# Performance work log

Hardware: AMD Instinct MI355X
Metric: run time of the kernel (lower is better)

The kernel has to match this reference:

```python
import jax, jax.numpy as jnp
import numpy as np

N, C, H, W = 4, 256, 64, 64
K, G, PAD, STRIDE, DIL = 3, 8, 1, 1, 1
GC = C // G      # channels per group
P = K * K        # sampling points per group
HIN, WIN = H + 2 * PAD, W + 2 * PAD
BN_EPS = 1e-5
LN_EPS = 1e-5


def setup_inputs():
    key = jax.random.key(0)
    ks = jax.random.split(key, 8)
    f32 = jnp.float32
    return {
        "x": jax.random.normal(ks[0], (N, C, H, W), dtype=f32),
        "w_in": jax.random.normal(ks[1], (C, C), dtype=f32) * 0.05,
        "b_in": jnp.zeros((C,), f32),
        "w_dw": jax.random.normal(ks[2], (C, 1, K, K), dtype=f32) * 0.1,
        "b_dw": jnp.zeros((C,), f32),
        "ln_g": jnp.ones((C,), f32), "ln_b": jnp.zeros((C,), f32),
        "w_off": jax.random.normal(ks[3], (C, G * P * 2), dtype=f32) * 0.01,
        "b_off": jax.random.normal(ks[4], (G * P * 2,), dtype=f32) * 0.01,
        "w_mask": jax.random.normal(ks[5], (C, G * P), dtype=f32) * 0.01,
        "b_mask": jnp.zeros((G * P,), f32),
        "w_out": jax.random.normal(ks[6], (C, C), dtype=f32) * 0.05,
        "b_out": jnp.zeros((C,), f32),
        "bn_g": jnp.ones((C,), f32), "bn_b": jnp.zeros((C,), f32),
        "bn_mean": jnp.zeros((C,), f32), "bn_var": jnp.ones((C,), f32),
    }


def _bilinear(img, grid):
    # img: (B, Cc, Hh, Ww); grid: (B, S, P, 2) normalized to [-1,1],
    # matches F.grid_sample(mode='bilinear', padding_mode='zeros', align_corners=False)
    B, Cc, Hh, Ww = img.shape
    gx = (grid[..., 0] + 1.0) * 0.5 * Ww - 0.5
    gy = (grid[..., 1] + 1.0) * 0.5 * Hh - 0.5
    x0 = jnp.floor(gx)
    y0 = jnp.floor(gy)
    wx = gx - x0
    wy = gy - y0
    flat = img.reshape(B, Cc, Hh * Ww)

    def tap(xi, yi, wgt):
        valid = (xi >= 0) & (xi <= Ww - 1) & (yi >= 0) & (yi <= Hh - 1)
        idx = (jnp.clip(yi, 0, Hh - 1) * Ww + jnp.clip(xi, 0, Ww - 1)).astype(jnp.int32)
        v = jax.vmap(lambda im, ix: im[:, ix])(flat, idx)   # (B, Cc, S, P)
        return v * (wgt * valid.astype(img.dtype))[:, None]

    return (tap(x0, y0, (1 - wx) * (1 - wy)) + tap(x0 + 1, y0, wx * (1 - wy))
            + tap(x0, y0 + 1, (1 - wx) * wy) + tap(x0 + 1, y0 + 1, wx * wy))


def _forward(x, w_in, b_in, w_dw, b_dw, ln_g, ln_b, w_off, b_off,
             w_mask, b_mask, w_out, b_out, bn_g, bn_b, bn_mean, bn_var):
    xl = jnp.transpose(x, (0, 2, 3, 1))                      # (N,H,W,C) channels-last
    x_proj = xl @ w_in + b_in                                # input_proj
    # depthwise conv + LayerNorm + GELU feature branch for offset/mask prediction
    dw = jax.lax.conv_general_dilated(
        x, w_dw, (1, 1), ((PAD, PAD), (PAD, PAD)),
        feature_group_count=C, dimension_numbers=("NCHW", "OIHW", "NCHW"))
    dw = jnp.transpose(dw + b_dw[None, :, None, None], (0, 2, 3, 1))
    mu = dw.mean(-1, keepdims=True)
    var = ((dw - mu) ** 2).mean(-1, keepdims=True)
    dw = (dw - mu) * jax.lax.rsqrt(var + LN_EPS) * ln_g + ln_b
    x1 = jax.nn.gelu(dw, approximate=False)
    offset = x1 @ w_off + b_off                              # (N,H,W,G*P*2)
    mask = jax.nn.softmax((x1 @ w_mask + b_mask).reshape(N, H, W, G, P), axis=-1)
    # reference points + dilation kernel grid, normalized to padded input, (x,y) order
    ry = ((DIL * (K - 1)) // 2 + 0.5 + jnp.arange(H, dtype=x.dtype) * STRIDE) / HIN
    rx = ((DIL * (K - 1)) // 2 + 0.5 + jnp.arange(W, dtype=x.dtype) * STRIDE) / WIN
    ref = jnp.stack(jnp.broadcast_arrays(rx[None, :], ry[:, None]), axis=-1)  # (H,W,2)
    px = (jnp.arange(K, dtype=x.dtype) * DIL - (DIL * (K - 1)) // 2) / WIN
    py = (jnp.arange(K, dtype=x.dtype) * DIL - (DIL * (K - 1)) // 2) / HIN
    gx, gy = jnp.meshgrid(px, py, indexing="ij")             # kw-major flattening as in DCNv3
    kgrid = jnp.stack([gx, gy], -1).reshape(P, 2)
    norm = jnp.array([WIN, HIN], dtype=x.dtype)
    loc = (ref[None, :, :, None, None, :] + kgrid[None, None, None, None, :, :]
           + offset.reshape(N, H, W, G, P, 2) / norm)        # (N,H,W,G,P,2), offset_scale=1
    sgrid = 2.0 * loc - 1.0
    # group-split padded value tensor and deformable sampling
    xp = jnp.pad(x_proj, ((0, 0), (PAD, PAD), (PAD, PAD), (0, 0)))
    img = jnp.transpose(xp, (0, 3, 1, 2)).reshape(N * G, GC, HIN, WIN)
    sg = jnp.transpose(sgrid.reshape(N, H * W, G, P, 2), (0, 2, 1, 3, 4)).reshape(N * G, H * W, P, 2)
    sampled = _bilinear(img, sg)                             # (N*G, GC, H*W, P)
    m = jnp.transpose(mask.reshape(N, H * W, G, P), (0, 2, 1, 3)).reshape(N * G, 1, H * W, P)
    agg = (sampled * m).sum(-1)                              # (N*G, GC, H*W)
    y = jnp.transpose(agg.reshape(N, C, H * W), (0, 2, 1)).reshape(N, H, W, C)
    y = y @ w_out + b_out                                    # output_proj
    y = jnp.transpose(y, (0, 3, 1, 2))                       # back to NCHW
    y = (y - bn_mean[None, :, None, None]) * jax.lax.rsqrt(bn_var + BN_EPS)[None, :, None, None]
    y = y * bn_g[None, :, None, None] + bn_b[None, :, None, None]
    return y * jax.nn.sigmoid(y)                             # SiLU (Conv.default_act)


def reference(x, w_in, b_in, w_dw, b_dw, ln_g, ln_b, w_off, b_off,
              w_mask, b_mask, w_out, b_out, bn_g, bn_b, bn_mean, bn_var):
    return _forward(x, w_in, b_in, w_dw, b_dw, ln_g, ln_b, w_off, b_off,
                    w_mask, b_mask, w_out, b_out, bn_g, bn_b, bn_mean, bn_var)
```

## Files before the change

kernel.cpp:

```cpp
#include <hip/hip_runtime.h>
#include <math.h>

#define NB   4
#define CCH  256
#define HH   64
#define WW   64
#define GG   8
#define GCH  32
#define PP   9
#define HIN  66
#define WIN  66
#define HWSZ 4096
#define NPIX 16384

#define XP_ELEMS   (NB*HIN*WIN*CCH)
#define AGG_ELEMS  (NPIX*CCH)
#define WINT_ELEMS (CCH*CCH)
#define WOUTT_ELEMS (CCH*CCH)
#define WOMT_ELEMS (216*CCH)
#define OFF_ELEMS  (NPIX*144)
#define MSK_ELEMS  (NPIX*72)

typedef __attribute__((ext_vector_type(8))) short bf16x8;
typedef __attribute__((ext_vector_type(4))) float f32x4;

__device__ __forceinline__ unsigned short f2bf(float f) {
    unsigned int u = __float_as_uint(f);
    unsigned int r = (u + 0x7FFFu + ((u >> 16) & 1u)) >> 16;
    return (unsigned short)r;
}
__device__ __forceinline__ float bf2f(unsigned short s) {
    return __uint_as_float(((unsigned int)s) << 16);
}

#define SDW_STRIDE 258

__global__ __launch_bounds__(256) void k_prep(
    const float* __restrict__ w_in, const float* __restrict__ w_off,
    const float* __restrict__ w_mask, const float* __restrict__ w_out,
    unsigned short* __restrict__ win_t, unsigned short* __restrict__ womt,
    unsigned short* __restrict__ wout_t, unsigned short* __restrict__ xp)
{
    const int gtid = blockIdx.x * 256 + threadIdx.x;
    const int STRIDE = 128 * 256;
    for (int i = gtid; i < 252928; i += STRIDE) {
        if (i < 65536) {
            int n = i & 255, k = i >> 8;
            win_t[n * 256 + k] = f2bf(w_in[i]);
        } else if (i < 131072) {
            int j = i - 65536;
            int n = j & 255, k = j >> 8;
            wout_t[n * 256 + k] = f2bf(w_out[j]);
        } else if (i < 186368) {
            int j = i - 131072;
            int k = j / 216, col = j - k * 216;
            float v = (col < 144) ? w_off[k * 144 + col]
                                  : w_mask[k * 72 + col - 144];
            womt[col * 256 + k] = f2bf(v);
        } else {
            int r = i - 186368;
            int seg = r >> 6, ln = r & 63;
            int n = seg / 260, rp = seg % 260;
            int h, w;
            if (rp < 66)       { h = 0;        w = rp; }
            else if (rp < 132) { h = 65;       w = rp - 66; }
            else if (rp < 196) { h = rp - 131; w = 0; }
            else               { h = rp - 195; w = 65; }
            uint2 z = make_uint2(0u, 0u);
            *(uint2*)&xp[(((size_t)n * HIN + h) * WIN + w) * CCH + ln * 4] = z;
        }
    }
}

__global__ __launch_bounds__(1024) void k_dw_fused(
    const float* __restrict__ x, const float* __restrict__ w_dw,
    const float* __restrict__ b_dw, const float* __restrict__ ln_g,
    const float* __restrict__ ln_b, const float* __restrict__ b_in,
    const unsigned short* __restrict__ win_t, const unsigned short* __restrict__ womt,
    const float* __restrict__ b_off, const float* __restrict__ b_mask,
    unsigned short* __restrict__ xp, float* __restrict__ off,
    float* __restrict__ msk)
{
    __shared__ unsigned short sdw[64 * SDW_STRIDE];
    __shared__ unsigned short sxr[64 * SDW_STRIDE];
    __shared__ float r1s[16][64];
    __shared__ float r2s[16][64];
    __shared__ float mu_s[64];
    __shared__ float rs_s[64];

    const int b = blockIdx.x;
    const int tid = threadIdx.x;
    const int h = b & 63;
    const int n = b >> 6;
    const int wave = __builtin_amdgcn_readfirstlane(tid >> 6);
    const int lane = tid & 63;

    const float* xn = x + (size_t)n * CCH * HWSZ;
    const bool h0ok = (h > 0);
    const bool h2ok = (h < HH - 1);

    float s1 = 0.f, s2 = 0.f;

#pragma unroll 4
    for (int it = 0; it < 16; it++) {
        const int c = it * 16 + wave;
        const float* xc = xn + (size_t)c * HWSZ + h * WW + lane;
        float v0 = h0ok ? xc[-WW] : 0.f;
        float v1 = xc[0];
        float v2 = h2ok ? xc[WW] : 0.f;

        const float* wk = w_dw + c * 9;
        float acc = b_dw[c];

        float l0 = __shfl_up(v0, 1);   if (lane == 0)  l0 = 0.f;
        float r0 = __shfl_down(v0, 1); if (lane == 63) r0 = 0.f;
        acc += wk[0] * l0 + wk[1] * v0 + wk[2] * r0;

        float l1 = __shfl_up(v1, 1);   if (lane == 0)  l1 = 0.f;
        float r1 = __shfl_down(v1, 1); if (lane == 63) r1 = 0.f;
        acc += wk[3] * l1 + wk[4] * v1 + wk[5] * r1;

        float l2 = __shfl_up(v2, 1);   if (lane == 0)  l2 = 0.f;
        float r2 = __shfl_down(v2, 1); if (lane == 63) r2 = 0.f;
        acc += wk[6] * l2 + wk[7] * v2 + wk[8] * r2;

        s1 += acc;
        s2 += acc * acc;
        sdw[lane * SDW_STRIDE + c] = f2bf(acc);
        sxr[lane * SDW_STRIDE + c] = f2bf(v1);
    }

    r1s[wave][lane] = s1;
    r2s[wave][lane] = s2;
    __syncthreads();

    if (tid < 64) {
        float a1 = 0.f, a2 = 0.f;
#pragma unroll
        for (int q = 0; q < 16; q++) { a1 += r1s[q][tid]; a2 += r2s[q][tid]; }
        float mu = a1 * (1.0f / 256.0f);
        float var = a2 * (1.0f / 256.0f) - mu * mu;
        mu_s[tid] = mu;
        rs_s[tid] = rsqrtf(var + 1e-5f);
    }
    __syncthreads();

    {
        const int c0 = (tid & 63) * 4;
        float g4[4], b4[4];
#pragma unroll
        for (int i = 0; i < 4; i++) { g4[i] = ln_g[c0 + i]; b4[i] = ln_b[c0 + i]; }
#pragma unroll
        for (int pass = 0; pass < 4; pass++) {
            int w = wave + pass * 16;
            float mu = mu_s[w], rs = rs_s[w];
            unsigned short* row = &sdw[w * SDW_STRIDE + c0];
#pragma unroll
            for (int i = 0; i < 4; i++) {
                float v = (bf2f(row[i]) - mu) * rs * g4[i] + b4[i];
                row[i] = f2bf(0.5f * v * (1.0f + erff(v * 0.70710678118654752f)));
            }
        }
    }
    __syncthreads();

    const int r16  = lane & 15;
    const int quad = lane >> 4;
    const int wm   = wave >> 2;
    const int wn   = wave & 3;

#define LOAD_A(frag, basep, koff)                                   \
    {                                                               \
        const unsigned short* ap_ = (basep) + (koff);               \
        ((unsigned int*)&(frag))[0] = *(const unsigned int*)&ap_[0];\
        ((unsigned int*)&(frag))[1] = *(const unsigned int*)&ap_[2];\
        ((unsigned int*)&(frag))[2] = *(const unsigned int*)&ap_[4];\
        ((unsigned int*)&(frag))[3] = *(const unsigned int*)&ap_[6];\
    }

    {
        f32x4 acc[4];
#pragma unroll
        for (int i = 0; i < 4; i++) acc[i] = (f32x4){0.f, 0.f, 0.f, 0.f};
        const unsigned short* arow = &sxr[(wm * 16 + r16) * SDW_STRIDE];

#pragma unroll
        for (int k0 = 0; k0 < CCH; k0 += 32) {
            bf16x8 a;
            LOAD_A(a, arow, k0 + quad * 8);
#pragma unroll
            for (int i = 0; i < 4; i++) {
                int co = (wn * 4 + i) * 16 + r16;
                bf16x8 bfr = *(const bf16x8*)&win_t[(size_t)co * CCH + k0 + quad * 8];
                acc[i] = __builtin_amdgcn_mfma_f32_16x16x32_bf16(a, bfr, acc[i], 0, 0, 0);
            }
        }

        unsigned short* xprow = xp + (((size_t)n * HIN + (h + 1)) * WIN + 1) * CCH;
#pragma unroll
        for (int i = 0; i < 4; i++) {
            int co = (wn * 4 + i) * 16 + r16;
            float bias = b_in[co];
#pragma unroll
            for (int r = 0; r < 4; r++) {
                int w = wm * 16 + quad * 4 + r;
                xprow[(size_t)w * CCH + co] = f2bf(acc[i][r] + bias);
            }
        }
    }

    {
        f32x4 acc[4];
#pragma unroll
        for (int i = 0; i < 4; i++) acc[i] = (f32x4){0.f, 0.f, 0.f, 0.f};
        const unsigned short* arow = &sdw[(wm * 16 + r16) * SDW_STRIDE];

#pragma unroll
        for (int k0 = 0; k0 < CCH; k0 += 32) {
            bf16x8 a;
            LOAD_A(a, arow, k0 + quad * 8);
#pragma unroll
            for (int i = 0; i < 4; i++) {
                int col = (wn * 4 + i) * 16 + r16;
                int colc = (col < 216) ? col : 215;
                bf16x8 bfr = *(const bf16x8*)&womt[(size_t)colc * CCH + k0 + quad * 8];
                acc[i] = __builtin_amdgcn_mfma_f32_16x16x32_bf16(a, bfr, acc[i], 0, 0, 0);
            }
        }

        const int sbase = n * HWSZ + h * WW;
#pragma unroll
        for (int i = 0; i < 4; i++) {
            int col = (wn * 4 + i) * 16 + r16;
            if (col >= 216) continue;
            float bias = (col < 144) ? b_off[col] : b_mask[col - 144];
#pragma unroll
            for (int r = 0; r < 4; r++) {
                int w = wm * 16 + quad * 4 + r;
                int s = sbase + w;
                float v = acc[i][r] + bias;
                if (col < 144) off[(size_t)s * 144 + col] = v;
                else           msk[(size_t)s * 72 + col - 144] = v;
            }
        }
    }
#undef LOAD_A
}

__device__ __forceinline__ void acc8_tap(float* a, uint4 vv, float wgt) {
    a[0] += wgt * __uint_as_float(vv.x << 16);
    a[1] += wgt * __uint_as_float(vv.x & 0xffff0000u);
    a[2] += wgt * __uint_as_float(vv.y << 16);
    a[3] += wgt * __uint_as_float(vv.y & 0xffff0000u);
    a[4] += wgt * __uint_as_float(vv.z << 16);
    a[5] += wgt * __uint_as_float(vv.z & 0xffff0000u);
    a[6] += wgt * __uint_as_float(vv.w << 16);
    a[7] += wgt * __uint_as_float(vv.w & 0xffff0000u);
}

__global__ __launch_bounds__(256) void k_sample_agg(
    const unsigned short* __restrict__ xp, const float* __restrict__ off,
    const float* __restrict__ msk, unsigned short* __restrict__ agg)
{
    __shared__ float  sm[576];
    __shared__ int2   tco[576];
    __shared__ float4 twt[576];

    const int tid = threadIdx.x;
    const int s0 = blockIdx.x * 8;

    if (tid < 64) {
        const int pix = tid >> 3, g = tid & 7;
        const float* mskp = msk + (size_t)(s0 + pix) * 72 + g * 9;
        float e[9];
        float mx = -1e30f;
#pragma unroll
        for (int p = 0; p < PP; p++) { e[p] = mskp[p]; mx = fmaxf(mx, e[p]); }
        float sum = 0.f;
#pragma unroll
        for (int p = 0; p < PP; p++) { e[p] = __expf(e[p] - mx); sum += e[p]; }
        float rs = 1.0f / sum;
#pragma unroll
        for (int p = 0; p < PP; p++) sm[tid * 9 + p] = e[p] * rs;
    }
    __syncthreads();

    for (int idx = tid; idx < 576; idx += 256) {
        int pix = idx / 72;
        int rem = idx - pix * 72;
        int g = rem / 9;
        int p = rem - g * 9;
        int s = s0 + pix;
        int hw = s & 4095;
        int h = hw >> 6, w = hw & 63;
        const float* offp = off + (size_t)s * 144 + g * 18 + p * 2;
        float ox = offp[0], oy = offp[1];
        int i = p / 3, j = p - i * 3;
        float fx = (float)(w + i) + ox;
        float fy = (float)(h + j) + oy;
        float x0f = floorf(fx), y0f = floorf(fy);
        int x0 = (int)x0f, y0 = (int)y0f;
        float wx = fx - x0f, wy = fy - y0f;
        float m = sm[idx];
        float w00 = (1.f - wx) * (1.f - wy) * m;
        float w10 = wx * (1.f - wy) * m;
        float w01 = (1.f - wx) * wy * m;
        float w11 = wx * wy * m;
        int x1c = x0 + 1, y1c = y0 + 1;
        if (!((x0  >= 0) && (x0  < WIN))) { w00 = 0.f; w01 = 0.f; }
        if (!((x1c >= 0) && (x1c < WIN))) { w10 = 0.f; w11 = 0.f; }
        if (!((y0  >= 0) && (y0  < HIN))) { w00 = 0.f; w10 = 0.f; }
        if (!((y1c >= 0) && (y1c < HIN))) { w01 = 0.f; w11 = 0.f; }
        int cx0 = min(max(x0, 0), WIN - 1), cx1 = min(max(x1c, 0), WIN - 1);
        int cy0 = min(max(y0, 0), HIN - 1), cy1 = min(max(y1c, 0), HIN - 1);
        tco[idx] = make_int2(cx0 | (cx1 << 16), cy0 | (cy1 << 16));
        twt[idx] = make_float4(w00, w10, w01, w11);
    }
    __syncthreads();

    const int pix = tid >> 5;
    const int l5 = tid & 31;
    const int g = l5 >> 2, c8 = l5 & 3;
    const int s = s0 + pix;
    const int n = s >> 12;
    const unsigned short* base = xp + (size_t)n * HIN * WIN * CCH + g * GCH + c8 * 8;
    const int tbase = pix * 72 + g * 9;

    float a[8];
#pragma unroll
    for (int i = 0; i < 8; i++) a[i] = 0.f;

#pragma unroll
    for (int p = 0; p < PP; p++) {
        int2 cc = tco[tbase + p];
        float4 wt = twt[tbase + p];
        int cx0 = cc.x & 0xFFFF, cx1 = cc.x >> 16;
        int cy0 = cc.y & 0xFFFF, cy1 = cc.y >> 16;
        const unsigned short* r0 = base + (size_t)(cy0 * WIN) * CCH;
        const unsigned short* r1 = base + (size_t)(cy1 * WIN) * CCH;
        uint4 v00 = *(const uint4*)&r0[(size_t)cx0 * CCH];
        uint4 v10 = *(const uint4*)&r0[(size_t)cx1 * CCH];
        uint4 v01 = *(const uint4*)&r1[(size_t)cx0 * CCH];
        uint4 v11 = *(const uint4*)&r1[(size_t)cx1 * CCH];
        acc8_tap(a, v00, wt.x);
        acc8_tap(a, v10, wt.y);
        acc8_tap(a, v01, wt.z);
        acc8_tap(a, v11, wt.w);
    }

    uint4 o;
    o.x = (unsigned int)f2bf(a[0]) | ((unsigned int)f2bf(a[1]) << 16);
    o.y = (unsigned int)f2bf(a[2]) | ((unsigned int)f2bf(a[3]) << 16);
    o.z = (unsigned int)f2bf(a[4]) | ((unsigned int)f2bf(a[5]) << 16);
    o.w = (unsigned int)f2bf(a[6]) | ((unsigned int)f2bf(a[7]) << 16);
    *(uint4*)&agg[(size_t)s * CCH + g * GCH + c8 * 8] = o;
}

__global__ __launch_bounds__(256) void k_gemm_out(
    const unsigned short* __restrict__ agg, const unsigned short* __restrict__ wout_t,
    const float* __restrict__ b_out, const float* __restrict__ bn_g,
    const float* __restrict__ bn_b, const float* __restrict__ bn_mean,
    const float* __restrict__ bn_var, float* __restrict__ out)
{
    const int m0  = blockIdx.x * 128;
    const int co0 = blockIdx.y * 64;
    const int tid = threadIdx.x;
    const int n   = m0 >> 12;
    const int hw0 = m0 & 4095;

    const int wave = tid >> 6;
    const int lane = tid & 63;
    const int r16  = lane & 15;
    const int quad = lane >> 4;
    const int mw   = wave * 32;

    f32x4 acc[2][4];
#pragma unroll
    for (int i = 0; i < 2; i++)
#pragma unroll
        for (int j = 0; j < 4; j++) acc[i][j] = (f32x4){0.f, 0.f, 0.f, 0.f};

    const unsigned short* a0p = agg + (size_t)(m0 + mw + r16) * CCH + quad * 8;
    const unsigned short* a1p = a0p + 16 * CCH;

#pragma unroll
    for (int k0 = 0; k0 < CCH; k0 += 32) {
        bf16x8 a0 = *(const bf16x8*)&a0p[k0];
        bf16x8 a1 = *(const bf16x8*)&a1p[k0];
#pragma unroll
        for (int nt = 0; nt < 4; nt++) {
            bf16x8 bfr = *(const bf16x8*)&wout_t[(size_t)(co0 + nt * 16 + r16) * CCH + k0 + quad * 8];
            acc[0][nt] = __builtin_amdgcn_mfma_f32_16x16x32_bf16(a0, bfr, acc[0][nt], 0, 0, 0);
            acc[1][nt] = __builtin_amdgcn_mfma_f32_16x16x32_bf16(a1, bfr, acc[1][nt], 0, 0, 0);
        }
    }

#pragma unroll
    for (int nt = 0; nt < 4; nt++) {
        int co = co0 + nt * 16 + r16;
        float mean = bn_mean[co];
        float rstd = rsqrtf(bn_var[co] + 1e-5f);
        float gg = bn_g[co], bb = bn_b[co], bo = b_out[co];
#pragma unroll
        for (int mt = 0; mt < 2; mt++) {
            int hwb = hw0 + mw + mt * 16 + quad * 4;
            float tmp[4];
#pragma unroll
            for (int r = 0; r < 4; r++) {
                float y = acc[mt][nt][r] + bo;
                float yh = (y - mean) * rstd * gg + bb;
                tmp[r] = yh / (1.0f + __expf(-yh));
            }
            float4 v = make_float4(tmp[0], tmp[1], tmp[2], tmp[3]);
            *(float4*)&out[((size_t)n * CCH + co) * HWSZ + hwb] = v;
        }
    }
}

extern "C" void kernel_launch(void* const* d_in, const int* in_sizes, int n_in,
                              void* d_out, int out_size, void* d_ws, size_t ws_size,
                              hipStream_t stream)
{
    const float* x       = (const float*)d_in[0];
    const float* w_in    = (const float*)d_in[1];
    const float* b_in    = (const float*)d_in[2];
    const float* w_dw    = (const float*)d_in[3];
    const float* b_dw    = (const float*)d_in[4];
    const float* ln_g    = (const float*)d_in[5];
    const float* ln_b    = (const float*)d_in[6];
    const float* w_off   = (const float*)d_in[7];
    const float* b_off   = (const float*)d_in[8];
    const float* w_mask  = (const float*)d_in[9];
    const float* b_mask  = (const float*)d_in[10];
    const float* w_out   = (const float*)d_in[11];
    const float* b_out   = (const float*)d_in[12];
    const float* bn_g    = (const float*)d_in[13];
    const float* bn_b    = (const float*)d_in[14];
    const float* bn_mean = (const float*)d_in[15];
    const float* bn_var  = (const float*)d_in[16];
    float* out = (float*)d_out;

    unsigned short* xp     = (unsigned short*)d_ws;
    unsigned short* agg    = xp + XP_ELEMS;
    unsigned short* win_t  = agg + AGG_ELEMS;
    unsigned short* wout_t = win_t + WINT_ELEMS;
    unsigned short* womt   = wout_t + WOUTT_ELEMS;
    float* off = (float*)(womt + WOMT_ELEMS);
    float* msk = off + OFF_ELEMS;

    k_prep<<<dim3(128), 256, 0, stream>>>(w_in, w_off, w_mask, w_out,
                                          win_t, womt, wout_t, xp);
    k_dw_fused<<<dim3(256), 1024, 0, stream>>>(x, w_dw, b_dw, ln_g, ln_b, b_in,
                                               win_t, womt, b_off, b_mask,
                                               xp, off, msk);
    k_sample_agg<<<dim3(2048), 256, 0, stream>>>(xp, off, msk, agg);
    k_gemm_out<<<dim3(128, 4), 256, 0, stream>>>(agg, wout_t, b_out, bn_g, bn_b, bn_mean, bn_var, out);
}
```

Measured before the change: 178.1 us.

## Fuse all stages into one cooperative megakernel with grid syncs

Replaces the four kernel launches with one cooperative kernel of 256 blocks × 1024 threads. Grid-wide syncs separate weight prep, the depthwise/LN/projection stage and the sampling stage. Offsets, masks and aggregated features now stay in LDS per row, and the output GEMM runs in the same block, so the off/msk/agg global round trips and the launch gaps go away. In exchange, grid syncs add cost, occupancy is tied to the large LDS footprint, and the sampling stage runs with only 256 blocks instead of 2048.

```diff
diff --git a/kernel.cpp b/kernel.cpp
--- a/kernel.cpp
+++ b/kernel.cpp
@@ -1,5 +1,8 @@
 #include <hip/hip_runtime.h>
+#include <hip/hip_cooperative_groups.h>
 #include <math.h>
+
+namespace cg = cooperative_groups;
 
 #define NB   4
 #define CCH  256
@@ -14,12 +17,9 @@
 #define NPIX 16384
 
 #define XP_ELEMS   (NB*HIN*WIN*CCH)
-#define AGG_ELEMS  (NPIX*CCH)
 #define WINT_ELEMS (CCH*CCH)
+#define WOMT_ELEMS (216*CCH)
 #define WOUTT_ELEMS (CCH*CCH)
-#define WOMT_ELEMS (216*CCH)
-#define OFF_ELEMS  (NPIX*144)
-#define MSK_ELEMS  (NPIX*72)
 
 typedef __attribute__((ext_vector_type(8))) short bf16x8;
 typedef __attribute__((ext_vector_type(4))) float f32x4;
@@ -34,218 +34,7 @@
 }
 
 #define SDW_STRIDE 258
-
-__global__ __launch_bounds__(256) void k_prep(
-    const float* __restrict__ w_in, const float* __restrict__ w_off,
-    const float* __restrict__ w_mask, const float* __restrict__ w_out,
-    unsigned short* __restrict__ win_t, unsigned short* __restrict__ womt,
-    unsigned short* __restrict__ wout_t, unsigned short* __restrict__ xp)
-{
-    const int gtid = blockIdx.x * 256 + threadIdx.x;
-    const int STRIDE = 128 * 256;
-    for (int i = gtid; i < 252928; i += STRIDE) {
-        if (i < 65536) {
-            int n = i & 255, k = i >> 8;
-            win_t[n * 256 + k] = f2bf(w_in[i]);
-        } else if (i < 131072) {
-            int j = i - 65536;
-            int n = j & 255, k = j >> 8;
-            wout_t[n * 256 + k] = f2bf(w_out[j]);
-        } else if (i < 186368) {
-            int j = i - 131072;
-            int k = j / 216, col = j - k * 216;
-            float v = (col < 144) ? w_off[k * 144 + col]
-                                  : w_mask[k * 72 + col - 144];
-            womt[col * 256 + k] = f2bf(v);
-        } else {
-            int r = i - 186368;
-            int seg = r >> 6, ln = r & 63;
-            int n = seg / 260, rp = seg % 260;
-            int h, w;
-            if (rp < 66)       { h = 0;        w = rp; }
-            else if (rp < 132) { h = 65;       w = rp - 66; }
-            else if (rp < 196) { h = rp - 131; w = 0; }
-            else               { h = rp - 195; w = 65; }
-            uint2 z = make_uint2(0u, 0u);
-            *(uint2*)&xp[(((size_t)n * HIN + h) * WIN + w) * CCH + ln * 4] = z;
-        }
-    }
-}
-
-__global__ __launch_bounds__(1024) void k_dw_fused(
-    const float* __restrict__ x, const float* __restrict__ w_dw,
-    const float* __restrict__ b_dw, const float* __restrict__ ln_g,
-    const float* __restrict__ ln_b, const float* __restrict__ b_in,
-    const unsigned short* __restrict__ win_t, const unsigned short* __restrict__ womt,
-    const float* __restrict__ b_off, const float* __restrict__ b_mask,
-    unsigned short* __restrict__ xp, float* __restrict__ off,
-    float* __restrict__ msk)
-{
-    __shared__ unsigned short sdw[64 * SDW_STRIDE];
-    __shared__ unsigned short sxr[64 * SDW_STRIDE];
-    __shared__ float r1s[16][64];
-    __shared__ float r2s[16][64];
-    __shared__ float mu_s[64];
-    __shared__ float rs_s[64];
-
-    const int b = blockIdx.x;
-    const int tid = threadIdx.x;
-    const int h = b & 63;
-    const int n = b >> 6;
-    const int wave = __builtin_amdgcn_readfirstlane(tid >> 6);
-    const int lane = tid & 63;
-
-    const float* xn = x + (size_t)n * CCH * HWSZ;
-    const bool h0ok = (h > 0);
-    const bool h2ok = (h < HH - 1);
-
-    float s1 = 0.f, s2 = 0.f;
-
-#pragma unroll 4
-    for (int it = 0; it < 16; it++) {
-        const int c = it * 16 + wave;
-        const float* xc = xn + (size_t)c * HWSZ + h * WW + lane;
-        float v0 = h0ok ? xc[-WW] : 0.f;
-        float v1 = xc[0];
-        float v2 = h2ok ? xc[WW] : 0.f;
-
-        const float* wk = w_dw + c * 9;
-        float acc = b_dw[c];
-
-        float l0 = __shfl_up(v0, 1);   if (lane == 0)  l0 = 0.f;
-        float r0 = __shfl_down(v0, 1); if (lane == 63) r0 = 0.f;
-        acc += wk[0] * l0 + wk[1] * v0 + wk[2] * r0;
-
-        float l1 = __shfl_up(v1, 1);   if (lane == 0)  l1 = 0.f;
-        float r1 = __shfl_down(v1, 1); if (lane == 63) r1 = 0.f;
-        acc += wk[3] * l1 + wk[4] * v1 + wk[5] * r1;
-
-        float l2 = __shfl_up(v2, 1);   if (lane == 0)  l2 = 0.f;
-        float r2 = __shfl_down(v2, 1); if (lane == 63) r2 = 0.f;
-        acc += wk[6] * l2 + wk[7] * v2 + wk[8] * r2;
-
-        s1 += acc;
-        s2 += acc * acc;
-        sdw[lane * SDW_STRIDE + c] = f2bf(acc);
-        sxr[lane * SDW_STRIDE + c] = f2bf(v1);
-    }
-
-    r1s[wave][lane] = s1;
-    r2s[wave][lane] = s2;
-    __syncthreads();
-
-    if (tid < 64) {
-        float a1 = 0.f, a2 = 0.f;
-#pragma unroll
-        for (int q = 0; q < 16; q++) { a1 += r1s[q][tid]; a2 += r2s[q][tid]; }
-        float mu = a1 * (1.0f / 256.0f);
-        float var = a2 * (1.0f / 256.0f) - mu * mu;
-        mu_s[tid] = mu;
-        rs_s[tid] = rsqrtf(var + 1e-5f);
-    }
-    __syncthreads();
-
-    {
-        const int c0 = (tid & 63) * 4;
-        float g4[4], b4[4];
-#pragma unroll
-        for (int i = 0; i < 4; i++) { g4[i] = ln_g[c0 + i]; b4[i] = ln_b[c0 + i]; }
-#pragma unroll
-        for (int pass = 0; pass < 4; pass++) {
-            int w = wave + pass * 16;
-            float mu = mu_s[w], rs = rs_s[w];
-            unsigned short* row = &sdw[w * SDW_STRIDE + c0];
-#pragma unroll
-            for (int i = 0; i < 4; i++) {
-                float v = (bf2f(row[i]) - mu) * rs * g4[i] + b4[i];
-                row[i] = f2bf(0.5f * v * (1.0f + erff(v * 0.70710678118654752f)));
-            }
-        }
-    }
-    __syncthreads();
-
-    const int r16  = lane & 15;
-    const int quad = lane >> 4;
-    const int wm   = wave >> 2;
-    const int wn   = wave & 3;
-
-#define LOAD_A(frag, basep, koff)                                   \
-    {                                                               \
-        const unsigned short* ap_ = (basep) + (koff);               \
-        ((unsigned int*)&(frag))[0] = *(const unsigned int*)&ap_[0];\
-        ((unsigned int*)&(frag))[1] = *(const unsigned int*)&ap_[2];\
-        ((unsigned int*)&(frag))[2] = *(const unsigned int*)&ap_[4];\
-        ((unsigned int*)&(frag))[3] = *(const unsigned int*)&ap_[6];\
-    }
-
-    {
-        f32x4 acc[4];
-#pragma unroll
-        for (int i = 0; i < 4; i++) acc[i] = (f32x4){0.f, 0.f, 0.f, 0.f};
-        const unsigned short* arow = &sxr[(wm * 16 + r16) * SDW_STRIDE];
-
-#pragma unroll
-        for (int k0 = 0; k0 < CCH; k0 += 32) {
-            bf16x8 a;
-            LOAD_A(a, arow, k0 + quad * 8);
-#pragma unroll
-            for (int i = 0; i < 4; i++) {
-                int co = (wn * 4 + i) * 16 + r16;
-                bf16x8 bfr = *(const bf16x8*)&win_t[(size_t)co * CCH + k0 + quad * 8];
-                acc[i] = __builtin_amdgcn_mfma_f32_16x16x32_bf16(a, bfr, acc[i], 0, 0, 0);
-            }
-        }
-
-        unsigned short* xprow = xp + (((size_t)n * HIN + (h + 1)) * WIN + 1) * CCH;
-#pragma unroll
-        for (int i = 0; i < 4; i++) {
-            int co = (wn * 4 + i) * 16 + r16;
-            float bias = b_in[co];
-#pragma unroll
-            for (int r = 0; r < 4; r++) {
-                int w = wm * 16 + quad * 4 + r;
-                xprow[(size_t)w * CCH + co] = f2bf(acc[i][r] + bias);
-            }
-        }
-    }
-
-    {
-        f32x4 acc[4];
-#pragma unroll
-        for (int i = 0; i < 4; i++) acc[i] = (f32x4){0.f, 0.f, 0.f, 0.f};
-        const unsigned short* arow = &sdw[(wm * 16 + r16) * SDW_STRIDE];
-
-#pragma unroll
-        for (int k0 = 0; k0 < CCH; k0 += 32) {
-            bf16x8 a;
-            LOAD_A(a, arow, k0 + quad * 8);
-#pragma unroll
-            for (int i = 0; i < 4; i++) {
-                int col = (wn * 4 + i) * 16 + r16;
-                int colc = (col < 216) ? col : 215;
-                bf16x8 bfr = *(const bf16x8*)&womt[(size_t)colc * CCH + k0 + quad * 8];
-                acc[i] = __builtin_amdgcn_mfma_f32_16x16x32_bf16(a, bfr, acc[i], 0, 0, 0);
-            }
-        }
-
-        const int sbase = n * HWSZ + h * WW;
-#pragma unroll
-        for (int i = 0; i < 4; i++) {
-            int col = (wn * 4 + i) * 16 + r16;
-            if (col >= 216) continue;
-            float bias = (col < 144) ? b_off[col] : b_mask[col - 144];
-#pragma unroll
-            for (int r = 0; r < 4; r++) {
-                int w = wm * 16 + quad * 4 + r;
-                int s = sbase + w;
-                float v = acc[i][r] + bias;
-                if (col < 144) off[(size_t)s * 144 + col] = v;
-                else           msk[(size_t)s * 72 + col - 144] = v;
-            }
-        }
-    }
-#undef LOAD_A
-}
+#define AGG_STRIDE 258
 
 __device__ __forceinline__ void acc8_tap(float* a, uint4 vv, float wgt) {
     a[0] += wgt * __uint_as_float(vv.x << 16);
@@ -258,161 +47,368 @@
     a[7] += wgt * __uint_as_float(vv.w & 0xffff0000u);
 }
 
-__global__ __launch_bounds__(256) void k_sample_agg(
-    const unsigned short* __restrict__ xp, const float* __restrict__ off,
-    const float* __restrict__ msk, unsigned short* __restrict__ agg)
+__global__ __launch_bounds__(1024) void k_mega(
+    const float* __restrict__ x, const float* __restrict__ w_in,
+    const float* __restrict__ b_in, const float* __restrict__ w_dw,
+    const float* __restrict__ b_dw, const float* __restrict__ ln_g,
+    const float* __restrict__ ln_b, const float* __restrict__ w_off,
+    const float* __restrict__ b_off, const float* __restrict__ w_mask,
+    const float* __restrict__ b_mask, const float* __restrict__ w_out,
+    const float* __restrict__ b_out, const float* __restrict__ bn_g,
+    const float* __restrict__ bn_b, const float* __restrict__ bn_mean,
+    const float* __restrict__ bn_var, float* __restrict__ out,
+    unsigned short* __restrict__ xp, unsigned short* __restrict__ win_t,
+    unsigned short* __restrict__ womt, unsigned short* __restrict__ wout_t)
 {
-    __shared__ float  sm[576];
-    __shared__ int2   tco[576];
-    __shared__ float4 twt[576];
-
+    cg::grid_group gridg = cg::this_grid();
+
+    __shared__ __align__(16) unsigned char smem_raw[97536];
+    __shared__ float lds_off[64][146];
+    __shared__ float lds_msk[64][74];
+
+    unsigned short* sdw = (unsigned short*)smem_raw;
+    unsigned short* sxr = sdw + 64 * SDW_STRIDE;
+    float (*r1s)[64] = (float(*)[64])(smem_raw + 66048);
+    float (*r2s)[64] = (float(*)[64])(smem_raw + 70144);
+    float* mu_s = (float*)(smem_raw + 74240);
+    float* rs_s = (float*)(smem_raw + 74496);
+    unsigned short* agg_l = (unsigned short*)smem_raw;
+    float*  smx = (float*)(smem_raw + 33024);
+    int2*   tco = (int2*)(smem_raw + 42240);
+    float4* twt = (float4*)(smem_raw + 60672);
+
+    const int b = blockIdx.x;
     const int tid = threadIdx.x;
-    const int s0 = blockIdx.x * 8;
-
-    if (tid < 64) {
-        const int pix = tid >> 3, g = tid & 7;
-        const float* mskp = msk + (size_t)(s0 + pix) * 72 + g * 9;
-        float e[9];
-        float mx = -1e30f;
-#pragma unroll
-        for (int p = 0; p < PP; p++) { e[p] = mskp[p]; mx = fmaxf(mx, e[p]); }
-        float sum = 0.f;
-#pragma unroll
-        for (int p = 0; p < PP; p++) { e[p] = __expf(e[p] - mx); sum += e[p]; }
-        float rs = 1.0f / sum;
-#pragma unroll
-        for (int p = 0; p < PP; p++) sm[tid * 9 + p] = e[p] * rs;
+    const int h = b & 63;
+    const int n = b >> 6;
+
+    {
+        const int i = b * 1024 + tid;
+        if (i < 252928) {
+            if (i < 65536) {
+                int nn = i & 255, k = i >> 8;
+                win_t[nn * 256 + k] = f2bf(w_in[i]);
+            } else if (i < 131072) {
+                int j = i - 65536;
+                int nn = j & 255, k = j >> 8;
+                wout_t[nn * 256 + k] = f2bf(w_out[j]);
+            } else if (i < 186368) {
+                int j = i - 131072;
+                int k = j / 216, col = j - k * 216;
+                float v = (col < 144) ? w_off[k * 144 + col]
+                                      : w_mask[k * 72 + col - 144];
+                womt[col * 256 + k] = f2bf(v);
+            } else {
+                int r = i - 186368;
+                int seg = r >> 6, ln = r & 63;
+                int nn = seg / 260, rp = seg % 260;
+                int hh, ww;
+                if (rp < 66)       { hh = 0;        ww = rp; }
+                else if (rp < 132) { hh = 65;       ww = rp - 66; }
+                else if (rp < 196) { hh = rp - 131; ww = 0; }
+                else               { hh = rp - 195; ww = 65; }
+                uint2 z = make_uint2(0u, 0u);
+                *(uint2*)&xp[(((size_t)nn * HIN + hh) * WIN + ww) * CCH + ln * 4] = z;
+            }
+        }
+    }
+    gridg.sync();
+
+    {
+        const int wave = __builtin_amdgcn_readfirstlane(tid >> 6);
+        const int lane = tid & 63;
+
+        const float* xn = x + (size_t)n * CCH * HWSZ;
+        const bool h0ok = (h > 0);
+        const bool h2ok = (h < HH - 1);
+
+        float s1 = 0.f, s2 = 0.f;
+
+#pragma unroll 4
+        for (int it = 0; it < 16; it++) {
+            const int c = it * 16 + wave;
+            const float* xc = xn + (size_t)c * HWSZ + h * WW + lane;
+            float v0 = h0ok ? xc[-WW] : 0.f;
+            float v1 = xc[0];
+            float v2 = h2ok ? xc[WW] : 0.f;
+
+            const float* wk = w_dw + c * 9;
+            float acc = b_dw[c];
+
+            float l0 = __shfl_up(v0, 1);   if (lane == 0)  l0 = 0.f;
+            float r0 = __shfl_down(v0, 1); if (lane == 63) r0 = 0.f;
+            acc += wk[0] * l0 + wk[1] * v0 + wk[2] * r0;
+
+            float l1 = __shfl_up(v1, 1);   if (lane == 0)  l1 = 0.f;
+            float r1 = __shfl_down(v1, 1); if (lane == 63) r1 = 0.f;
+            acc += wk[3] * l1 + wk[4] * v1 + wk[5] * r1;
+
+            float l2 = __shfl_up(v2, 1);   if (lane == 0)  l2 = 0.f;
+            float r2 = __shfl_down(v2, 1); if (lane == 63) r2 = 0.f;
+            acc += wk[6] * l2 + wk[7] * v2 + wk[8] * r2;
+
+            s1 += acc;
+            s2 += acc * acc;
+            sdw[lane * SDW_STRIDE + c] = f2bf(acc);
+            sxr[lane * SDW_STRIDE + c] = f2bf(v1);
+        }
+
+        r1s[wave][lane] = s1;
+        r2s[wave][lane] = s2;
+        __syncthreads();
+
+        if (tid < 64) {
+            float a1 = 0.f, a2 = 0.f;
+#pragma unroll
+            for (int q = 0; q < 16; q++) { a1 += r1s[q][tid]; a2 += r2s[q][tid]; }
+            float mu = a1 * (1.0f / 256.0f);
+            float var = a2 * (1.0f / 256.0f) - mu * mu;
+            mu_s[tid] = mu;
+            rs_s[tid] = rsqrtf(var + 1e-5f);
+        }
+        __syncthreads();
+
+        {
+            const int c0 = (tid & 63) * 4;
+            float g4[4], b4[4];
+#pragma unroll
+            for (int i = 0; i < 4; i++) { g4[i] = ln_g[c0 + i]; b4[i] = ln_b[c0 + i]; }
+#pragma unroll
+            for (int pass = 0; pass < 4; pass++) {
+                int w = wave + pass * 16;
+                float mu = mu_s[w], rs = rs_s[w];
+                unsigned short* row = &sdw[w * SDW_STRIDE + c0];
+#pragma unroll
+                for (int i = 0; i < 4; i++) {
+                    float v = (bf2f(row[i]) - mu) * rs * g4[i] + b4[i];
+                    row[i] = f2bf(0.5f * v * (1.0f + erff(v * 0.70710678118654752f)));
+                }
+            }
+        }
+        __syncthreads();
+
+        const int r16  = lane & 15;
+        const int quad = lane >> 4;
+        const int wm   = wave >> 2;
+        const int wn   = wave & 3;
+
+#define LOAD_A(frag, basep, koff)                                   \
+        {                                                           \
+            const unsigned short* ap_ = (basep) + (koff);           \
+            ((unsigned int*)&(frag))[0] = *(const unsigned int*)&ap_[0];\
+            ((unsigned int*)&(frag))[1] = *(const unsigned int*)&ap_[2];\
+            ((unsigned int*)&(frag))[2] = *(const unsigned int*)&ap_[4];\
+            ((unsigned int*)&(frag))[3] = *(const unsigned int*)&ap_[6];\
+        }
+
+        {
+            f32x4 acc[4];
+#pragma unroll
+            for (int i = 0; i < 4; i++) acc[i] = (f32x4){0.f, 0.f, 0.f, 0.f};
+            const unsigned short* arow = &sxr[(wm * 16 + r16) * SDW_STRIDE];
+
+#pragma unroll
+            for (int k0 = 0; k0 < CCH; k0 += 32) {
+                bf16x8 a;
+                LOAD_A(a, arow, k0 + quad * 8);
+#pragma unroll
+                for (int i = 0; i < 4; i++) {
+                    int co = (wn * 4 + i) * 16 + r16;
+                    bf16x8 bfr = *(const bf16x8*)&win_t[(size_t)co * CCH + k0 + quad * 8];
+                    acc[i] = __builtin_amdgcn_mfma_f32_16x16x32_bf16(a, bfr, acc[i], 0, 0, 0);
+                }
+            }
+
+            unsigned short* xprow = xp + (((size_t)n * HIN + (h + 1)) * WIN + 1) * CCH;
+#pragma unroll
+            for (int i = 0; i < 4; i++) {
+                int co = (wn * 4 + i) * 16 + r16;
+                float bias = b_in[co];
+#pragma unroll
+                for (int r = 0; r < 4; r++) {
+                    int w = wm * 16 + quad * 4 + r;
+                    xprow[(size_t)w * CCH + co] = f2bf(acc[i][r] + bias);
+                }
+            }
+        }
+
+        {
+            f32x4 acc[4];
+#pragma unroll
+            for (int i = 0; i < 4; i++) acc[i] = (f32x4){0.f, 0.f, 0.f, 0.f};
+            const unsigned short* arow = &sdw[(wm * 16 + r16) * SDW_STRIDE];
+
+#pragma unroll
+            for (int k0 = 0; k0 < CCH; k0 += 32) {
+                bf16x8 a;
+                LOAD_A(a, arow, k0 + quad * 8);
+#pragma unroll
+                for (int i = 0; i < 4; i++) {
+                    int col = (wn * 4 + i) * 16 + r16;
+                    int colc = (col < 216) ? col : 215;
+                    bf16x8 bfr = *(const bf16x8*)&womt[(size_t)colc * CCH + k0 + quad * 8];
+                    acc[i] = __builtin_amdgcn_mfma_f32_16x16x32_bf16(a, bfr, acc[i], 0, 0, 0);
+                }
+            }
+
+#pragma unroll
+            for (int i = 0; i < 4; i++) {
+                int col = (wn * 4 + i) * 16 + r16;
+                if (col >= 216) continue;
+                float bias = (col < 144) ? b_off[col] : b_mask[col - 144];
+#pragma unroll
+                for (int r = 0; r < 4; r++) {
+                    int w = wm * 16 + quad * 4 + r;
+                    float v = acc[i][r] + bias;
+                    if (col < 144) lds_off[w][col] = v;
+                    else           lds_msk[w][col - 144] = v;
+                }
+            }
+        }
+    }
+    gridg.sync();
+
+    {
+        const int sub  = tid >> 8;
+        const int stid = tid & 255;
+        float*  smg = &smx[sub * 576];
+        int2*   tcg = &tco[sub * 576];
+        float4* twg = &twt[sub * 576];
+
+        for (int chunk = 0; chunk < 2; ++chunk) {
+            __syncthreads();
+            const int lp0 = chunk * 32 + sub * 8;
+
+            if (stid < 64) {
+                const int pix = stid >> 3, g = stid & 7;
+                const float* mskp = &lds_msk[lp0 + pix][g * 9];
+                float e[9];
+                float mx = -1e30f;
+#pragma unroll
+                for (int p = 0; p < PP; p++) { e[p] = mskp[p]; mx = fmaxf(mx, e[p]); }
+                float sum = 0.f;
+#pragma unroll
+                for (int p = 0; p < PP; p++) { e[p] = __expf(e[p] - mx); sum += e[p]; }
+                float rs = 1.0f / sum;
+#pragma unroll
+                for (int p = 0; p < PP; p++) smg[stid * 9 + p] = e[p] * rs;
+            }
+            __syncthreads();
+
+            for (int idx = stid; idx < 576; idx += 256) {
+                int pix = idx / 72;
+                int rem = idx - pix * 72;
+                int g = rem / 9;
+                int p = rem - g * 9;
+                int lp = lp0 + pix;
+                int w = lp;
+                const float* offp = &lds_off[lp][g * 18 + p * 2];
+                float ox = offp[0], oy = offp[1];
+                int i = p / 3, j = p - i * 3;
+                float fx = (float)(w + i) + ox;
+                float fy = (float)(h + j) + oy;
+                float x0f = floorf(fx), y0f = floorf(fy);
+                int x0 = (int)x0f, y0 = (int)y0f;
+                float wx = fx - x0f, wy = fy - y0f;
+                float m = smg[idx];
+                float w00 = (1.f - wx) * (1.f - wy) * m;
+                float w10 = wx * (1.f - wy) * m;
+                float w01 = (1.f - wx) * wy * m;
+                float w11 = wx * wy * m;
+                int x1c = x0 + 1, y1c = y0 + 1;
+                if (!((x0  >= 0) && (x0  < WIN))) { w00 = 0.f; w01 = 0.f; }
+                if (!((x1c >= 0) && (x1c < WIN))) { w10 = 0.f; w11 = 0.f; }
+                if (!((y0  >= 0) && (y0  < HIN))) { w00 = 0.f; w10 = 0.f; }
+                if (!((y1c >= 0) && (y1c < HIN))) { w01 = 0.f; w11 = 0.f; }
+                int cx0 = min(max(x0, 0), WIN - 1), cx1 = min(max(x1c, 0), WIN - 1);
+                int cy0 = min(max(y0, 0), HIN - 1), cy1 = min(max(y1c, 0), HIN - 1);
+                tcg[idx] = make_int2(cx0 | (cx1 << 16), cy0 | (cy1 << 16));
+                twg[idx] = make_float4(w00, w10, w01, w11);
+            }
+            __syncthreads();
+
+            {
+                const int pix = stid >> 5;
+                const int l5 = stid & 31;
+                const int g = l5 >> 2, c8 = l5 & 3;
+                const int lp = lp0 + pix;
+                const unsigned short* base = xp + (size_t)n * HIN * WIN * CCH + g * GCH + c8 * 8;
+                const int tbase = pix * 72 + g * 9;
+
+                float a[8];
+#pragma unroll
+                for (int i = 0; i < 8; i++) a[i] = 0.f;
+
+#pragma unroll
+                for (int p = 0; p < PP; p++) {
+                    int2 cc = tcg[tbase + p];
+                    float4 wt = twg[tbase + p];
+                    int cx0 = cc.x & 0xFFFF, cx1 = cc.x >> 16;
+                    int cy0 = cc.y & 0xFFFF, cy1 = cc.y >> 16;
+                    const unsigned short* r0 = base + (size_t)(cy0 * WIN) * CCH;
+                    const unsigned short* r1 = base + (size_t)(cy1 * WIN) * CCH;
+                    uint4 v00 = *(const uint4*)&r0[(size_t)cx0 * CCH];
+                    uint4 v10 = *(const uint4*)&r0[(size_t)cx1 * CCH];
+                    uint4 v01 = *(const uint4*)&r1[(size_t)cx0 * CCH];
+                    uint4 v11 = *(const uint4*)&r1[(size_t)cx1 * CCH];
+                    acc8_tap(a, v00, wt.x);
+                    acc8_tap(a, v10, wt.y);
+                    acc8_tap(a, v01, wt.z);
+                    acc8_tap(a, v11, wt.w);
+                }
+
+                unsigned int* dst = (unsigned int*)&agg_l[lp * AGG_STRIDE + g * GCH + c8 * 8];
+                dst[0] = (unsigned int)f2bf(a[0]) | ((unsigned int)f2bf(a[1]) << 16);
+                dst[1] = (unsigned int)f2bf(a[2]) | ((unsigned int)f2bf(a[3]) << 16);
+                dst[2] = (unsigned int)f2bf(a[4]) | ((unsigned int)f2bf(a[5]) << 16);
+                dst[3] = (unsigned int)f2bf(a[6]) | ((unsigned int)f2bf(a[7]) << 16);
+            }
+        }
     }
     __syncthreads();
 
-    for (int idx = tid; idx < 576; idx += 256) {
-        int pix = idx / 72;
-        int rem = idx - pix * 72;
-        int g = rem / 9;
-        int p = rem - g * 9;
-        int s = s0 + pix;
-        int hw = s & 4095;
-        int h = hw >> 6, w = hw & 63;
-        const float* offp = off + (size_t)s * 144 + g * 18 + p * 2;
-        float ox = offp[0], oy = offp[1];
-        int i = p / 3, j = p - i * 3;
-        float fx = (float)(w + i) + ox;
-        float fy = (float)(h + j) + oy;
-        float x0f = floorf(fx), y0f = floorf(fy);
-        int x0 = (int)x0f, y0 = (int)y0f;
-        float wx = fx - x0f, wy = fy - y0f;
-        float m = sm[idx];
-        float w00 = (1.f - wx) * (1.f - wy) * m;
-        float w10 = wx * (1.f - wy) * m;
-        float w01 = (1.f - wx) * wy * m;
-        float w11 = wx * wy * m;
-        int x1c = x0 + 1, y1c = y0 + 1;
-        if (!((x0  >= 0) && (x0  < WIN))) { w00 = 0.f; w01 = 0.f; }
-        if (!((x1c >= 0) && (x1c < WIN))) { w10 = 0.f; w11 = 0.f; }
-        if (!((y0  >= 0) && (y0  < HIN))) { w00 = 0.f; w10 = 0.f; }
-        if (!((y1c >= 0) && (y1c < HIN))) { w01 = 0.f; w11 = 0.f; }
-        int cx0 = min(max(x0, 0), WIN - 1), cx1 = min(max(x1c, 0), WIN - 1);
-        int cy0 = min(max(y0, 0), HIN - 1), cy1 = min(max(y1c, 0), HIN - 1);
-        tco[idx] = make_int2(cx0 | (cx1 << 16), cy0 | (cy1 << 16));
-        twt[idx] = make_float4(w00, w10, w01, w11);
-    }
-    __syncthreads();
-
-    const int pix = tid >> 5;
-    const int l5 = tid & 31;
-    const int g = l5 >> 2, c8 = l5 & 3;
-    const int s = s0 + pix;
-    const int n = s >> 12;
-    const unsigned short* base = xp + (size_t)n * HIN * WIN * CCH + g * GCH + c8 * 8;
-    const int tbase = pix * 72 + g * 9;
-
-    float a[8];
-#pragma unroll
-    for (int i = 0; i < 8; i++) a[i] = 0.f;
-
-#pragma unroll
-    for (int p = 0; p < PP; p++) {
-        int2 cc = tco[tbase + p];
-        float4 wt = twt[tbase + p];
-        int cx0 = cc.x & 0xFFFF, cx1 = cc.x >> 16;
-        int cy0 = cc.y & 0xFFFF, cy1 = cc.y >> 16;
-        const unsigned short* r0 = base + (size_t)(cy0 * WIN) * CCH;
-        const unsigned short* r1 = base + (size_t)(cy1 * WIN) * CCH;
-        uint4 v00 = *(const uint4*)&r0[(size_t)cx0 * CCH];
-        uint4 v10 = *(const uint4*)&r0[(size_t)cx1 * CCH];
-        uint4 v01 = *(const uint4*)&r1[(size_t)cx0 * CCH];
-        uint4 v11 = *(const uint4*)&r1[(size_t)cx1 * CCH];
-        acc8_tap(a, v00, wt.x);
-        acc8_tap(a, v10, wt.y);
-        acc8_tap(a, v01, wt.z);
-        acc8_tap(a, v11, wt.w);
-    }
-
-    uint4 o;
-    o.x = (unsigned int)f2bf(a[0]) | ((unsigned int)f2bf(a[1]) << 16);
-    o.y = (unsigned int)f2bf(a[2]) | ((unsigned int)f2bf(a[3]) << 16);
-    o.z = (unsigned int)f2bf(a[4]) | ((unsigned int)f2bf(a[5]) << 16);
-    o.w = (unsigned int)f2bf(a[6]) | ((unsigned int)f2bf(a[7]) << 16);
-    *(uint4*)&agg[(size_t)s * CCH + g * GCH + c8 * 8] = o;
-}
-
-__global__ __launch_bounds__(256) void k_gemm_out(
-    const unsigned short* __restrict__ agg, const unsigned short* __restrict__ wout_t,
-    const float* __restrict__ b_out, const float* __restrict__ bn_g,
-    const float* __restrict__ bn_b, const float* __restrict__ bn_mean,
-    const float* __restrict__ bn_var, float* __restrict__ out)
-{
-    const int m0  = blockIdx.x * 128;
-    const int co0 = blockIdx.y * 64;
-    const int tid = threadIdx.x;
-    const int n   = m0 >> 12;
-    const int hw0 = m0 & 4095;
-
-    const int wave = tid >> 6;
-    const int lane = tid & 63;
-    const int r16  = lane & 15;
-    const int quad = lane >> 4;
-    const int mw   = wave * 32;
-
-    f32x4 acc[2][4];
-#pragma unroll
-    for (int i = 0; i < 2; i++)
-#pragma unroll
-        for (int j = 0; j < 4; j++) acc[i][j] = (f32x4){0.f, 0.f, 0.f, 0.f};
-
-    const unsigned short* a0p = agg + (size_t)(m0 + mw + r16) * CCH + quad * 8;
-    const unsigned short* a1p = a0p + 16 * CCH;
-
-#pragma unroll
-    for (int k0 = 0; k0 < CCH; k0 += 32) {
-        bf16x8 a0 = *(const bf16x8*)&a0p[k0];
-        bf16x8 a1 = *(const bf16x8*)&a1p[k0];
+    {
+        const int wave = tid >> 6;
+        const int lane = tid & 63;
+        const int r16  = lane & 15;
+        const int quad = lane >> 4;
+        const int wm   = wave >> 2;
+        const int wn   = wave & 3;
+
+        f32x4 acc[4];
+#pragma unroll
+        for (int i = 0; i < 4; i++) acc[i] = (f32x4){0.f, 0.f, 0.f, 0.f};
+
+        const unsigned short* arow = &agg_l[(wm * 16 + r16) * AGG_STRIDE];
+
+#pragma unroll
+        for (int k0 = 0; k0 < CCH; k0 += 32) {
+            bf16x8 a;
+            LOAD_A(a, arow, k0 + quad * 8);
+#pragma unroll
+            for (int nt = 0; nt < 4; nt++) {
+                int co = wn * 64 + nt * 16 + r16;
+                bf16x8 bfr = *(const bf16x8*)&wout_t[(size_t)co * CCH + k0 + quad * 8];
+                acc[nt] = __builtin_amdgcn_mfma_f32_16x16x32_bf16(a, bfr, acc[nt], 0, 0, 0);
+            }
+        }
+#undef LOAD_A
+
 #pragma unroll
         for (int nt = 0; nt < 4; nt++) {
-            bf16x8 bfr = *(const bf16x8*)&wout_t[(size_t)(co0 + nt * 16 + r16) * CCH + k0 + quad * 8];
-            acc[0][nt] = __builtin_amdgcn_mfma_f32_16x16x32_bf16(a0, bfr, acc[0][nt], 0, 0, 0);
-            acc[1][nt] = __builtin_amdgcn_mfma_f32_16x16x32_bf16(a1, bfr, acc[1][nt], 0, 0, 0);
-        }
-    }
-
-#pragma unroll
-    for (int nt = 0; nt < 4; nt++) {
-        int co = co0 + nt * 16 + r16;
-        float mean = bn_mean[co];
-        float rstd = rsqrtf(bn_var[co] + 1e-5f);
-        float gg = bn_g[co], bb = bn_b[co], bo = b_out[co];
-#pragma unroll
-        for (int mt = 0; mt < 2; mt++) {
-            int hwb = hw0 + mw + mt * 16 + quad * 4;
+            int co = wn * 64 + nt * 16 + r16;
+            float mean = bn_mean[co];
+            float rstd = rsqrtf(bn_var[co] + 1e-5f);
+            float gg = bn_g[co], bb = bn_b[co], bo = b_out[co];
             float tmp[4];
 #pragma unroll
             for (int r = 0; r < 4; r++) {
-                float y = acc[mt][nt][r] + bo;
+                float y = acc[nt][r] + bo;
                 float yh = (y - mean) * rstd * gg + bb;
                 tmp[r] = yh / (1.0f + __expf(-yh));
             }
             float4 v = make_float4(tmp[0], tmp[1], tmp[2], tmp[3]);
-            *(float4*)&out[((size_t)n * CCH + co) * HWSZ + hwb] = v;
+            *(float4*)&out[((size_t)n * CCH + co) * HWSZ + h * WW + wm * 16 + quad * 4] = v;
         }
     }
 }
@@ -441,18 +437,17 @@
     float* out = (float*)d_out;
 
     unsigned short* xp     = (unsigned short*)d_ws;
-    unsigned short* agg    = xp + XP_ELEMS;
-    unsigned short* win_t  = agg + AGG_ELEMS;
-    unsigned short* wout_t = win_t + WINT_ELEMS;
-    unsigned short* womt   = wout_t + WOUTT_ELEMS;
-    float* off = (float*)(womt + WOMT_ELEMS);
-    float* msk = off + OFF_ELEMS;
-
-    k_prep<<<dim3(128), 256, 0, stream>>>(w_in, w_off, w_mask, w_out,
-                                          win_t, womt, wout_t, xp);
-    k_dw_fused<<<dim3(256), 1024, 0, stream>>>(x, w_dw, b_dw, ln_g, ln_b, b_in,
-                                               win_t, womt, b_off, b_mask,
-                                               xp, off, msk);
-    k_sample_agg<<<dim3(2048), 256, 0, stream>>>(xp, off, msk, agg);
-    k_gemm_out<<<dim3(128, 4), 256, 0, stream>>>(agg, wout_t, b_out, bn_g, bn_b, bn_mean, bn_var, out);
+    unsigned short* win_t  = xp + XP_ELEMS;
+    unsigned short* womt   = win_t + WINT_ELEMS;
+    unsigned short* wout_t = womt + WOMT_ELEMS;
+
+    void* args[] = {
+        (void*)&x, (void*)&w_in, (void*)&b_in, (void*)&w_dw, (void*)&b_dw,
+        (void*)&ln_g, (void*)&ln_b, (void*)&w_off, (void*)&b_off,
+        (void*)&w_mask, (void*)&b_mask, (void*)&w_out, (void*)&b_out,
+        (void*)&bn_g, (void*)&bn_b, (void*)&bn_mean, (void*)&bn_var,
+        (void*)&out, (void*)&xp, (void*)&win_t, (void*)&womt, (void*)&wout_t
+    };
+    hipLaunchCooperativeKernel((const void*)k_mega, dim3(256), dim3(1024),
+                               args, 0, stream);
 }
```

Measured after the change: 271.4 us. 1.52x slower.
